# Kernel optimization log

Measured on AMD Instinct MI355X. Metric: run time of the kernel, lower is better.

The kernel has to match this reference:

```python
import jax, jax.numpy as jnp
import numpy as np

B, S, D, H = 2, 2048, 1024, 16
DK = D // H


def setup_inputs() -> dict:
    key = jax.random.key(0)
    ks = jax.random.split(key, 7)
    q = jax.random.normal(ks[0], (B, S, D), dtype=jnp.float32)
    k = jax.random.normal(ks[1], (B, S, D), dtype=jnp.float32)
    v = jax.random.normal(ks[2], (B, S, D), dtype=jnp.float32)
    # causal mask: mask==0 positions get -1e9 before softmax
    mask = jnp.tril(jnp.ones((S, S), dtype=jnp.int32))[None, None, :, :]
    scale = 0.02
    w_q = jax.random.normal(ks[3], (D, D), dtype=jnp.float32) * scale
    w_k = jax.random.normal(ks[4], (D, D), dtype=jnp.float32) * scale
    w_v = jax.random.normal(ks[5], (D, D), dtype=jnp.float32) * scale
    w_o = jax.random.normal(ks[6], (D, D), dtype=jnp.float32) * scale
    return {"q": q, "k": k, "v": v, "mask": mask,
            "w_q": w_q, "w_k": w_k, "w_v": w_v, "w_o": w_o}


def reference(q, k, v, mask, w_q, w_k, w_v, w_o):
    # nn.Linear(bias=False): x @ W.T
    query = q @ w_q.T  # [B,S,D]
    key = k @ w_k.T
    value = v @ w_v.T
    # split heads -> [B,H,S,DK]
    query = query.reshape(B, S, H, DK).transpose(0, 2, 1, 3)
    key = key.reshape(B, S, H, DK).transpose(0, 2, 1, 3)
    value = value.reshape(B, S, H, DK).transpose(0, 2, 1, 3)
    scores = jnp.einsum('bhqd,bhkd->bhqk', query, key) / jnp.sqrt(
        jnp.asarray(DK, dtype=query.dtype))
    scores = jnp.where(mask == 0, jnp.asarray(-1e9, scores.dtype), scores)
    attn = jax.nn.softmax(scores, axis=-1)  # dropout p=0.0 -> identity
    x = jnp.einsum('bhqk,bhkd->bhqd', attn, value)  # [B,H,S,DK]
    x = x.transpose(0, 2, 1, 3).reshape(B, S, D)
    return x @ w_o.T
```

## Files before the change

kernel.cpp:

```cpp
#include <hip/hip_runtime.h>

typedef __attribute__((ext_vector_type(8))) short short8;
typedef __attribute__((ext_vector_type(4))) float f32x4;

#define DEVI static __device__ __forceinline__

constexpr int BB = 2, SS = 2048, DD = 1024, HH = 16, DKK = 64;
constexpr size_t QN = (size_t)BB * SS * DD;
constexpr size_t WN = (size_t)DD * DD;

constexpr size_t OFF_WQ = 3 * QN;
constexpr size_t OFF_WO = OFF_WQ + 3 * WN;
constexpr size_t OFF_QM = OFF_WQ + 4 * WN;
constexpr size_t OFF_KM = OFF_QM + QN;
constexpr size_t OFF_VM = OFF_QM + 2 * QN;
constexpr size_t OFF_XC = OFF_QM + 3 * QN;

DEVI unsigned short f2bf(float f) {
  unsigned int u = __float_as_uint(f);
  u = (u + 0x7fffu + ((u >> 16) & 1u)) >> 16;
  return (unsigned short)u;
}

DEVI f32x4 fzero() { f32x4 z = {0.f, 0.f, 0.f, 0.f}; return z; }

DEVI void gld16(const void* g, void* l) {
  __builtin_amdgcn_global_load_lds((__attribute__((address_space(1))) void*)g,
                                   (__attribute__((address_space(3))) void*)l,
                                   16, 0, 0);
}

DEVI short8 mk8u(unsigned int a, unsigned int b, unsigned int c, unsigned int d) {
  union { short8 s; unsigned int u[4]; } x;
  x.u[0] = a; x.u[1] = b; x.u[2] = c; x.u[3] = d;
  return x.s;
}

DEVI short8 mk8q(unsigned long long lo, unsigned long long hi) {
  union { short8 s; unsigned long long q[2]; } x;
  x.q[0] = lo; x.q[1] = hi;
  return x.s;
}

DEVI unsigned int pkbf(float a, float b) {
  return __builtin_amdgcn_perm(__float_as_uint(b), __float_as_uint(a), 0x07060302u);
}

__global__ __launch_bounds__(256) void convert_all(
    const float* __restrict__ q, const float* __restrict__ k,
    const float* __restrict__ v, const float* __restrict__ wq,
    const float* __restrict__ wk, const float* __restrict__ wv,
    const float* __restrict__ wo, unsigned short* __restrict__ ws) {
  size_t t = (size_t)blockIdx.x * 256 + threadIdx.x;
  size_t e = t * 4;
  const float* src;
  size_t base, idx;
  if (e < 3 * QN) {
    size_t a = e >> 22;
    idx = e & (QN - 1);
    src = (a == 0) ? q : (a == 1) ? k : v;
    base = a * QN;
  } else {
    size_t r = e - 3 * QN;
    size_t a = r >> 20;
    idx = r & (WN - 1);
    src = (a == 0) ? wq : (a == 1) ? wk : (a == 2) ? wv : wo;
    base = 3 * QN + a * WN;
  }
  float4 f = *(const float4*)(src + idx);
  ushort4 o;
  o.x = f2bf(f.x); o.y = f2bf(f.y); o.z = f2bf(f.z); o.w = f2bf(f.w);
  *(ushort4*)(ws + base + idx) = o;
}

DEVI void gemm_tile_db(const unsigned short* __restrict__ A,
                       const unsigned short* __restrict__ Bw,
                       unsigned short* ldsA, unsigned short* ldsB,
                       int m0, int n0, f32x4 acc[4][4]) {
  const int tid = threadIdx.x;
  const int w = tid >> 6, l = tid & 63;
  const int lr = l & 15, qd = l >> 4;
  const int wr = w >> 1, wc = w & 1;

#pragma unroll
  for (int i = 0; i < 4; ++i)
#pragma unroll
    for (int j = 0; j < 4; ++j) acc[i][j] = fzero();

  const unsigned short* pa[4];
  const unsigned short* pb[4];
  int ls[4];
#pragma unroll
  for (int u = 0; u < 4; ++u) {
    int s = w * 4 + u;
    int t16 = s >> 1, kt = s & 1;
    pa[u] = A + (size_t)(m0 + t16 * 16 + lr) * DD + kt * 32 + qd * 8;
    pb[u] = Bw + (size_t)(n0 + t16 * 16 + lr) * DD + kt * 32 + qd * 8;
    ls[u] = s * 512;
  }

#pragma unroll
  for (int u = 0; u < 4; ++u) gld16(pa[u], ldsA + ls[u]);
#pragma unroll
  for (int u = 0; u < 4; ++u) gld16(pb[u], ldsB + ls[u]);

  constexpr int NIT = DD / 64;
#pragma unroll 1
  for (int it = 0; it < NIT; ++it) {
    __syncthreads();
    const int cur = (it & 1) * 8192;
    const int nxt = 8192 - cur;
    if (it + 1 < NIT) {
      const int k1 = (it + 1) * 64;
#pragma unroll
      for (int u = 0; u < 4; ++u) gld16(pa[u] + k1, ldsA + nxt + ls[u]);
#pragma unroll
      for (int u = 0; u < 4; ++u) gld16(pb[u] + k1, ldsB + nxt + ls[u]);
    }
#pragma unroll
    for (int ks = 0; ks < 2; ++ks) {
      short8 af[4], bf[4];
#pragma unroll
      for (int im = 0; im < 4; ++im)
        af[im] = *(const short8*)&ldsA[cur + ((wr * 4 + im) * 2 + ks) * 512 + l * 8];
#pragma unroll
      for (int in = 0; in < 4; ++in)
        bf[in] = *(const short8*)&ldsB[cur + ((wc * 4 + in) * 2 + ks) * 512 + l * 8];
#pragma unroll
      for (int im = 0; im < 4; ++im)
#pragma unroll
        for (int in = 0; in < 4; ++in)
          acc[im][in] = __builtin_amdgcn_mfma_f32_16x16x32_bf16(
              af[im], bf[in], acc[im][in], 0, 0, 0);
    }
  }
}

DEVI void gemm64_db(const unsigned short* __restrict__ A,
                    const unsigned short* __restrict__ Bw,
                    unsigned short* ldsA, unsigned short* ldsB,
                    int m0, int n0, f32x4 acc[4][2]) {
  const int tid = threadIdx.x;
  const int w = tid >> 6, l = tid & 63;
  const int lr = l & 15, qd = l >> 4;

#pragma unroll
  for (int i = 0; i < 4; ++i)
#pragma unroll
    for (int j = 0; j < 2; ++j) acc[i][j] = fzero();

  const unsigned short* pa[2];
  const unsigned short* pb[4];
  int lsa[2], lsb[4];
#pragma unroll
  for (int kh = 0; kh < 2; ++kh) {
    pa[kh] = A + (size_t)(m0 + w * 16 + lr) * DD + kh * 32 + qd * 8;
    lsa[kh] = (w * 2 + kh) * 512;
  }
#pragma unroll
  for (int r = 0; r < 2; ++r)
#pragma unroll
    for (int kh = 0; kh < 2; ++kh) {
      pb[r * 2 + kh] = Bw + (size_t)(n0 + (2 * w + r) * 16 + lr) * DD + kh * 32 + qd * 8;
      lsb[r * 2 + kh] = ((2 * w + r) * 2 + kh) * 512;
    }

#pragma unroll
  for (int u = 0; u < 2; ++u) gld16(pa[u], ldsA + lsa[u]);
#pragma unroll
  for (int u = 0; u < 4; ++u) gld16(pb[u], ldsB + lsb[u]);

  constexpr int NIT = DD / 64;
#pragma unroll 1
  for (int it = 0; it < NIT; ++it) {
    __syncthreads();
    const int curA = (it & 1) * 4096, curB = (it & 1) * 8192;
    if (it + 1 < NIT) {
      const int k1 = (it + 1) * 64;
      const int nxtA = 4096 - curA, nxtB = 8192 - curB;
#pragma unroll
      for (int u = 0; u < 2; ++u) gld16(pa[u] + k1, ldsA + nxtA + lsa[u]);
#pragma unroll
      for (int u = 0; u < 4; ++u) gld16(pb[u] + k1, ldsB + nxtB + lsb[u]);
    }
#pragma unroll
    for (int ks = 0; ks < 2; ++ks) {
      short8 af[4], bf[2];
#pragma unroll
      for (int im = 0; im < 4; ++im)
        af[im] = *(const short8*)&ldsA[curA + (im * 2 + ks) * 512 + l * 8];
#pragma unroll
      for (int in = 0; in < 2; ++in)
        bf[in] = *(const short8*)&ldsB[curB + ((2 * w + in) * 2 + ks) * 512 + l * 8];
#pragma unroll
      for (int im = 0; im < 4; ++im)
#pragma unroll
        for (int in = 0; in < 2; ++in)
          acc[im][in] = __builtin_amdgcn_mfma_f32_16x16x32_bf16(
              af[im], bf[in], acc[im][in], 0, 0, 0);
    }
  }
}

__global__ __launch_bounds__(256) void proj_gemm(unsigned short* __restrict__ ws) {
  __shared__ unsigned short ldsA[16384];
  __shared__ unsigned short ldsB[16384];
  const int z = blockIdx.z;
  const unsigned short* A = ws + (size_t)z * QN;
  const unsigned short* W = ws + OFF_WQ + (size_t)z * WN;
  unsigned short* O = ws + OFF_QM + (size_t)z * QN;
  const int m0 = blockIdx.x * 128, n0 = blockIdx.y * 128;
  f32x4 acc[4][4];
  gemm_tile_db(A, W, ldsA, ldsB, m0, n0, acc);

  const int tid = threadIdx.x;
  const int w = tid >> 6, l = tid & 63, lr = l & 15, qd = l >> 4;
  const int wr = w >> 1, wc = w & 1;
  if (z == 2) {
#pragma unroll
    for (int im = 0; im < 4; ++im)
#pragma unroll
      for (int in = 0; in < 4; ++in) {
        const int n = n0 + wc * 64 + in * 16 + lr;
        const int h = n >> 6, dk = n & 63;
        const int m = m0 + wr * 64 + im * 16 + qd * 4;
        const int b = m >> 11, s = m & 2047;
        ushort4 pk;
        pk.x = f2bf(acc[im][in][0]); pk.y = f2bf(acc[im][in][1]);
        pk.z = f2bf(acc[im][in][2]); pk.w = f2bf(acc[im][in][3]);
        *(ushort4*)&O[((size_t)(b * HH + h) * DKK + dk) * SS + s] = pk;
      }
  } else {
#pragma unroll
    for (int im = 0; im < 4; ++im)
#pragma unroll
      for (int in = 0; in < 4; ++in) {
        const int n = n0 + wc * 64 + in * 16 + lr;
        const int h = n >> 6, dk = n & 63;
#pragma unroll
        for (int i = 0; i < 4; ++i) {
          const int m = m0 + wr * 64 + im * 16 + qd * 4 + i;
          const int b = m >> 11, s = m & 2047;
          O[((size_t)(b * HH + h) * SS + s) * DKK + dk] = f2bf(acc[im][in][i]);
        }
      }
  }
}

__global__ __launch_bounds__(512) void flash_attn(
    const unsigned short* __restrict__ Qm, const unsigned short* __restrict__ Km,
    const unsigned short* __restrict__ Vt, unsigned short* __restrict__ Xc) {
  __shared__ unsigned short Kl[2][4096];
  __shared__ unsigned short Vl[2][4096];
  const int p = blockIdx.x, head = blockIdx.y, b = blockIdx.z;
  const int tid = threadIdx.x, w = tid >> 6, l = tid & 63, lr = l & 15, qd = l >> 4;
  const size_t bh = (size_t)(b * HH + head);
  const unsigned short* Qb = Qm + bh * SS * DKK;
  const unsigned short* Kb = Km + bh * SS * DKK;
  const unsigned short* Vb = Vt + bh * DKK * SS;

  const bool heavy = (w < 4);
  const int qt = heavy ? (31 - p) : p;
  const int nkv = 32 - p;
  const int qrow = qt * 64 + (w & 3) * 16 + lr;

  const int s0 = heavy ? w : (w - 4);
  const int s1 = s0 + 4;
  const int loOff = ((qd >> 1) * 16 + lr) * 8 + (qd & 1) * 4;
  const int hiOff = ((2 + (qd >> 1)) * 16 + lr) * 8 + (qd & 1) * 4;

  short8 qf0 = *(const short8*)&Qb[(size_t)qrow * DKK + qd * 8];
  short8 qf1 = *(const short8*)&Qb[(size_t)qrow * DKK + 32 + qd * 8];

  f32x4 o[4];
#pragma unroll
  for (int i = 0; i < 4; ++i) o[i] = fzero();
  float ll = 0.f;
  const float c1 = 0.18033688011112042f;
  const float mc = 8.0f * c1;

  {
    if (heavy) {
      gld16(&Kb[(size_t)((s0 >> 1) * 16 + lr) * DKK + (s0 & 1) * 32 + qd * 8],
            &Kl[0][s0 * 512]);
      gld16(&Kb[(size_t)((s1 >> 1) * 16 + lr) * DKK + (s1 & 1) * 32 + qd * 8],
            &Kl[0][s1 * 512]);
    } else {
      gld16(&Vb[(size_t)((s0 >> 1) * 16 + lr) * SS + (s0 & 1) * 32 + qd * 8],
            &Vl[0][s0 * 512]);
      gld16(&Vb[(size_t)((s1 >> 1) * 16 + lr) * SS + (s1 & 1) * 32 + qd * 8],
            &Vl[0][s1 * 512]);
    }
  }

#pragma unroll 1
  for (int kv = 0; kv < nkv; ++kv) {
    __syncthreads();
    const int cur = kv & 1;
    if (kv + 1 < nkv) {
      const int kv0n = (kv + 1) * 64;
      if (heavy) {
        gld16(&Kb[(size_t)(kv0n + (s0 >> 1) * 16 + lr) * DKK + (s0 & 1) * 32 + qd * 8],
              &Kl[cur ^ 1][s0 * 512]);
        gld16(&Kb[(size_t)(kv0n + (s1 >> 1) * 16 + lr) * DKK + (s1 & 1) * 32 + qd * 8],
              &Kl[cur ^ 1][s1 * 512]);
      } else {
        gld16(&Vb[(size_t)((s0 >> 1) * 16 + lr) * SS + kv0n + (s0 & 1) * 32 + qd * 8],
              &Vl[cur ^ 1][s0 * 512]);
        gld16(&Vb[(size_t)((s1 >> 1) * 16 + lr) * SS + kv0n + (s1 & 1) * 32 + qd * 8],
              &Vl[cur ^ 1][s1 * 512]);
      }
    }

    if (kv <= qt) {
      const int kv0 = kv * 64;
      f32x4 sc[4];
#pragma unroll
      for (int nt = 0; nt < 4; ++nt) {
        short8 kf0 = *(const short8*)&Kl[cur][(nt * 2 + 0) * 512 + l * 8];
        short8 kf1 = *(const short8*)&Kl[cur][(nt * 2 + 1) * 512 + l * 8];
        f32x4 zz = fzero();
        zz = __builtin_amdgcn_mfma_f32_16x16x32_bf16(kf0, qf0, zz, 0, 0, 0);
        sc[nt] = __builtin_amdgcn_mfma_f32_16x16x32_bf16(kf1, qf1, zz, 0, 0, 0);
      }
      if (kv == qt) {
#pragma unroll
        for (int nt = 0; nt < 4; ++nt)
#pragma unroll
          for (int i = 0; i < 4; ++i) {
            const int kvi = kv0 + nt * 16 + qd * 4 + i;
            if (kvi > qrow) sc[nt][i] = -3e38f;
          }
      }

      float rs = 0.f;
#pragma unroll
      for (int nt = 0; nt < 4; ++nt)
#pragma unroll
        for (int i = 0; i < 4; ++i) {
          const float pp = exp2f(fmaf(sc[nt][i], c1, -mc));
          sc[nt][i] = pp;
          rs += pp;
        }
      rs += __shfl_xor(rs, 16);
      rs += __shfl_xor(rs, 32);
      ll += rs;

      unsigned int pd[4][2];
#pragma unroll
      for (int f = 0; f < 4; ++f) {
        pd[f][0] = pkbf(sc[f][0], sc[f][1]);
        pd[f][1] = pkbf(sc[f][2], sc[f][3]);
      }

#pragma unroll
      for (int kh = 0; kh < 2; ++kh) {
        short8 bfr = mk8u(pd[2 * kh][0], pd[2 * kh][1],
                          pd[2 * kh + 1][0], pd[2 * kh + 1][1]);
#pragma unroll
        for (int mt = 0; mt < 4; ++mt) {
          const int sbase = (mt * 2 + kh) * 512;
          const unsigned long long lo =
              *(const unsigned long long*)&Vl[cur][sbase + loOff];
          const unsigned long long hi =
              *(const unsigned long long*)&Vl[cur][sbase + hiOff];
          o[mt] = __builtin_amdgcn_mfma_f32_16x16x32_bf16(mk8q(lo, hi), bfr,
                                                          o[mt], 0, 0, 0);
        }
      }
    }
  }

  const float inv = 1.0f / ll;
  unsigned short* Xr = Xc + ((size_t)b * SS + qrow) * DD + (size_t)head * DKK;
#pragma unroll
  for (int mt = 0; mt < 4; ++mt)
#pragma unroll
    for (int i = 0; i < 4; ++i)
      Xr[mt * 16 + qd * 4 + i] = f2bf(o[mt][i] * inv);
}

__global__ __launch_bounds__(256) void out_gemm(
    const unsigned short* __restrict__ Xc, const unsigned short* __restrict__ Wo,
    float* __restrict__ out) {
  __shared__ unsigned short ldsA[8192];
  __shared__ unsigned short ldsB[16384];
  const int m0 = blockIdx.x * 64, n0 = blockIdx.y * 128;
  f32x4 acc[4][2];
  gemm64_db(Xc, Wo, ldsA, ldsB, m0, n0, acc);

  const int tid = threadIdx.x;
  const int w = tid >> 6, l = tid & 63, lr = l & 15, qd = l >> 4;
#pragma unroll
  for (int im = 0; im < 4; ++im)
#pragma unroll
    for (int in = 0; in < 2; ++in) {
      const int n = n0 + w * 32 + in * 16 + lr;
#pragma unroll
      for (int i = 0; i < 4; ++i) {
        const int m = m0 + im * 16 + qd * 4 + i;
        out[(size_t)m * DD + n] = acc[im][in][i];
      }
    }
}

extern "C" void kernel_launch(void* const* d_in, const int* in_sizes, int n_in,
                              void* d_out, int out_size, void* d_ws, size_t ws_size,
                              hipStream_t stream) {
  (void)in_sizes; (void)n_in; (void)out_size; (void)ws_size;
  const float* q  = (const float*)d_in[0];
  const float* k  = (const float*)d_in[1];
  const float* v  = (const float*)d_in[2];
  const float* wq = (const float*)d_in[4];
  const float* wk = (const float*)d_in[5];
  const float* wv = (const float*)d_in[6];
  const float* wo = (const float*)d_in[7];
  unsigned short* ws = (unsigned short*)d_ws;
  float* out = (float*)d_out;

  convert_all<<<dim3(16384), dim3(256), 0, stream>>>(q, k, v, wq, wk, wv, wo, ws);
  proj_gemm<<<dim3(32, 8, 3), dim3(256), 0, stream>>>(ws);
  flash_attn<<<dim3(16, 16, 2), dim3(512), 0, stream>>>(ws + OFF_QM, ws + OFF_KM,
                                                        ws + OFF_VM, ws + OFF_XC);
  out_gemm<<<dim3(64, 8), dim3(256), 0, stream>>>(ws + OFF_XC, ws + OFF_WO, out);
}
```

Baseline: 252.6 us.

## Pair heavy/light query tiles per wave in flash attention; XCD-aware GEMM block remap

Attention blocks drop from 512 to 256 threads. Each wave now handles both a heavy (late) and a light (early) query tile, sharing each K/V LDS tile between the two MFMA streams instead of assigning them to separate waves. This balances causal work across waves and reuses K/V fragment loads, at the cost of higher register pressure and every wave loading both K and V. The projection and output GEMMs are also launched as 1D grids with an XCD-aware index remap, so blocks sharing A rows land on the same XCD for better L2 reuse.

```diff
diff --git a/kernel.cpp b/kernel.cpp
--- a/kernel.cpp
+++ b/kernel.cpp
@@ -205,11 +205,15 @@
 __global__ __launch_bounds__(256) void proj_gemm(unsigned short* __restrict__ ws) {
   __shared__ unsigned short ldsA[16384];
   __shared__ unsigned short ldsB[16384];
-  const int z = blockIdx.z;
+  const int idx = blockIdx.x;
+  const int z = idx >> 8;
+  const int r = idx & 255;
+  const int xcd = r & 7, t = r >> 3;
+  const int m0 = (xcd + 8 * (t & 3)) * 128;
+  const int n0 = (t >> 2) * 128;
   const unsigned short* A = ws + (size_t)z * QN;
   const unsigned short* W = ws + OFF_WQ + (size_t)z * WN;
   unsigned short* O = ws + OFF_QM + (size_t)z * QN;
-  const int m0 = blockIdx.x * 128, n0 = blockIdx.y * 128;
   f32x4 acc[4][4];
   gemm_tile_db(A, W, ldsA, ldsB, m0, n0, acc);
 
@@ -247,7 +251,7 @@
   }
 }
 
-__global__ __launch_bounds__(512) void flash_attn(
+__global__ __launch_bounds__(256) void flash_attn(
     const unsigned short* __restrict__ Qm, const unsigned short* __restrict__ Km,
     const unsigned short* __restrict__ Vt, unsigned short* __restrict__ Xc) {
   __shared__ unsigned short Kl[2][4096];
@@ -259,38 +263,36 @@
   const unsigned short* Kb = Km + bh * SS * DKK;
   const unsigned short* Vb = Vt + bh * DKK * SS;
 
-  const bool heavy = (w < 4);
-  const int qt = heavy ? (31 - p) : p;
+  const int qt_h = 31 - p;
   const int nkv = 32 - p;
-  const int qrow = qt * 64 + (w & 3) * 16 + lr;
-
-  const int s0 = heavy ? w : (w - 4);
-  const int s1 = s0 + 4;
+  const int qrow_h = qt_h * 64 + w * 16 + lr;
+  const int qrow_l = p * 64 + w * 16 + lr;
+
+  const int s0 = w, s1 = w + 4;
   const int loOff = ((qd >> 1) * 16 + lr) * 8 + (qd & 1) * 4;
   const int hiOff = ((2 + (qd >> 1)) * 16 + lr) * 8 + (qd & 1) * 4;
 
-  short8 qf0 = *(const short8*)&Qb[(size_t)qrow * DKK + qd * 8];
-  short8 qf1 = *(const short8*)&Qb[(size_t)qrow * DKK + 32 + qd * 8];
-
-  f32x4 o[4];
-#pragma unroll
-  for (int i = 0; i < 4; ++i) o[i] = fzero();
-  float ll = 0.f;
+  short8 qh0 = *(const short8*)&Qb[(size_t)qrow_h * DKK + qd * 8];
+  short8 qh1 = *(const short8*)&Qb[(size_t)qrow_h * DKK + 32 + qd * 8];
+  short8 ql0 = *(const short8*)&Qb[(size_t)qrow_l * DKK + qd * 8];
+  short8 ql1 = *(const short8*)&Qb[(size_t)qrow_l * DKK + 32 + qd * 8];
+
+  f32x4 oh[4], ol[4];
+#pragma unroll
+  for (int i = 0; i < 4; ++i) { oh[i] = fzero(); ol[i] = fzero(); }
+  float lh = 0.f, lt = 0.f;
   const float c1 = 0.18033688011112042f;
   const float mc = 8.0f * c1;
 
   {
-    if (heavy) {
-      gld16(&Kb[(size_t)((s0 >> 1) * 16 + lr) * DKK + (s0 & 1) * 32 + qd * 8],
-            &Kl[0][s0 * 512]);
-      gld16(&Kb[(size_t)((s1 >> 1) * 16 + lr) * DKK + (s1 & 1) * 32 + qd * 8],
-            &Kl[0][s1 * 512]);
-    } else {
-      gld16(&Vb[(size_t)((s0 >> 1) * 16 + lr) * SS + (s0 & 1) * 32 + qd * 8],
-            &Vl[0][s0 * 512]);
-      gld16(&Vb[(size_t)((s1 >> 1) * 16 + lr) * SS + (s1 & 1) * 32 + qd * 8],
-            &Vl[0][s1 * 512]);
-    }
+    gld16(&Kb[(size_t)((s0 >> 1) * 16 + lr) * DKK + (s0 & 1) * 32 + qd * 8],
+          &Kl[0][s0 * 512]);
+    gld16(&Kb[(size_t)((s1 >> 1) * 16 + lr) * DKK + (s1 & 1) * 32 + qd * 8],
+          &Kl[0][s1 * 512]);
+    gld16(&Vb[(size_t)((s0 >> 1) * 16 + lr) * SS + (s0 & 1) * 32 + qd * 8],
+          &Vl[0][s0 * 512]);
+    gld16(&Vb[(size_t)((s1 >> 1) * 16 + lr) * SS + (s1 & 1) * 32 + qd * 8],
+          &Vl[0][s1 * 512]);
   }
 
 #pragma unroll 1
@@ -299,64 +301,102 @@
     const int cur = kv & 1;
     if (kv + 1 < nkv) {
       const int kv0n = (kv + 1) * 64;
-      if (heavy) {
-        gld16(&Kb[(size_t)(kv0n + (s0 >> 1) * 16 + lr) * DKK + (s0 & 1) * 32 + qd * 8],
-              &Kl[cur ^ 1][s0 * 512]);
-        gld16(&Kb[(size_t)(kv0n + (s1 >> 1) * 16 + lr) * DKK + (s1 & 1) * 32 + qd * 8],
-              &Kl[cur ^ 1][s1 * 512]);
-      } else {
-        gld16(&Vb[(size_t)((s0 >> 1) * 16 + lr) * SS + kv0n + (s0 & 1) * 32 + qd * 8],
-              &Vl[cur ^ 1][s0 * 512]);
-        gld16(&Vb[(size_t)((s1 >> 1) * 16 + lr) * SS + kv0n + (s1 & 1) * 32 + qd * 8],
-              &Vl[cur ^ 1][s1 * 512]);
-      }
-    }
-
-    if (kv <= qt) {
-      const int kv0 = kv * 64;
-      f32x4 sc[4];
+      gld16(&Kb[(size_t)(kv0n + (s0 >> 1) * 16 + lr) * DKK + (s0 & 1) * 32 + qd * 8],
+            &Kl[cur ^ 1][s0 * 512]);
+      gld16(&Kb[(size_t)(kv0n + (s1 >> 1) * 16 + lr) * DKK + (s1 & 1) * 32 + qd * 8],
+            &Kl[cur ^ 1][s1 * 512]);
+      gld16(&Vb[(size_t)((s0 >> 1) * 16 + lr) * SS + kv0n + (s0 & 1) * 32 + qd * 8],
+            &Vl[cur ^ 1][s0 * 512]);
+      gld16(&Vb[(size_t)((s1 >> 1) * 16 + lr) * SS + kv0n + (s1 & 1) * 32 + qd * 8],
+            &Vl[cur ^ 1][s1 * 512]);
+    }
+
+    const int kv0 = kv * 64;
+    const bool lite = (kv <= p);
+    f32x4 sh[4], sl[4];
+    if (lite) {
 #pragma unroll
       for (int nt = 0; nt < 4; ++nt) {
         short8 kf0 = *(const short8*)&Kl[cur][(nt * 2 + 0) * 512 + l * 8];
         short8 kf1 = *(const short8*)&Kl[cur][(nt * 2 + 1) * 512 + l * 8];
-        f32x4 zz = fzero();
-        zz = __builtin_amdgcn_mfma_f32_16x16x32_bf16(kf0, qf0, zz, 0, 0, 0);
-        sc[nt] = __builtin_amdgcn_mfma_f32_16x16x32_bf16(kf1, qf1, zz, 0, 0, 0);
-      }
-      if (kv == qt) {
-#pragma unroll
-        for (int nt = 0; nt < 4; ++nt)
-#pragma unroll
-          for (int i = 0; i < 4; ++i) {
-            const int kvi = kv0 + nt * 16 + qd * 4 + i;
-            if (kvi > qrow) sc[nt][i] = -3e38f;
-          }
-      }
-
+        f32x4 z0 = __builtin_amdgcn_mfma_f32_16x16x32_bf16(kf0, qh0, fzero(), 0, 0, 0);
+        sh[nt] = __builtin_amdgcn_mfma_f32_16x16x32_bf16(kf1, qh1, z0, 0, 0, 0);
+        f32x4 z1 = __builtin_amdgcn_mfma_f32_16x16x32_bf16(kf0, ql0, fzero(), 0, 0, 0);
+        sl[nt] = __builtin_amdgcn_mfma_f32_16x16x32_bf16(kf1, ql1, z1, 0, 0, 0);
+      }
+    } else {
+#pragma unroll
+      for (int nt = 0; nt < 4; ++nt) {
+        short8 kf0 = *(const short8*)&Kl[cur][(nt * 2 + 0) * 512 + l * 8];
+        short8 kf1 = *(const short8*)&Kl[cur][(nt * 2 + 1) * 512 + l * 8];
+        f32x4 z0 = __builtin_amdgcn_mfma_f32_16x16x32_bf16(kf0, qh0, fzero(), 0, 0, 0);
+        sh[nt] = __builtin_amdgcn_mfma_f32_16x16x32_bf16(kf1, qh1, z0, 0, 0, 0);
+      }
+    }
+
+    if (kv == qt_h) {
+#pragma unroll
+      for (int nt = 0; nt < 4; ++nt)
+#pragma unroll
+        for (int i = 0; i < 4; ++i)
+          if (kv0 + nt * 16 + qd * 4 + i > qrow_h) sh[nt][i] = -3e38f;
+    }
+
+    unsigned int pdh[4][2];
+    {
       float rs = 0.f;
 #pragma unroll
       for (int nt = 0; nt < 4; ++nt)
 #pragma unroll
         for (int i = 0; i < 4; ++i) {
-          const float pp = exp2f(fmaf(sc[nt][i], c1, -mc));
-          sc[nt][i] = pp;
+          const float pp = exp2f(fmaf(sh[nt][i], c1, -mc));
+          sh[nt][i] = pp;
           rs += pp;
         }
       rs += __shfl_xor(rs, 16);
       rs += __shfl_xor(rs, 32);
-      ll += rs;
-
-      unsigned int pd[4][2];
+      lh += rs;
 #pragma unroll
       for (int f = 0; f < 4; ++f) {
-        pd[f][0] = pkbf(sc[f][0], sc[f][1]);
-        pd[f][1] = pkbf(sc[f][2], sc[f][3]);
-      }
-
+        pdh[f][0] = pkbf(sh[f][0], sh[f][1]);
+        pdh[f][1] = pkbf(sh[f][2], sh[f][3]);
+      }
+    }
+    unsigned int pdl[4][2];
+    if (lite) {
+      if (kv == p) {
+#pragma unroll
+        for (int nt = 0; nt < 4; ++nt)
+#pragma unroll
+          for (int i = 0; i < 4; ++i)
+            if (kv0 + nt * 16 + qd * 4 + i > qrow_l) sl[nt][i] = -3e38f;
+      }
+      float rs = 0.f;
+#pragma unroll
+      for (int nt = 0; nt < 4; ++nt)
+#pragma unroll
+        for (int i = 0; i < 4; ++i) {
+          const float pp = exp2f(fmaf(sl[nt][i], c1, -mc));
+          sl[nt][i] = pp;
+          rs += pp;
+        }
+      rs += __shfl_xor(rs, 16);
+      rs += __shfl_xor(rs, 32);
+      lt += rs;
+#pragma unroll
+      for (int f = 0; f < 4; ++f) {
+        pdl[f][0] = pkbf(sl[f][0], sl[f][1]);
+        pdl[f][1] = pkbf(sl[f][2], sl[f][3]);
+      }
+    }
+
+    if (lite) {
 #pragma unroll
       for (int kh = 0; kh < 2; ++kh) {
-        short8 bfr = mk8u(pd[2 * kh][0], pd[2 * kh][1],
-                          pd[2 * kh + 1][0], pd[2 * kh + 1][1]);
+        short8 bh_ = mk8u(pdh[2 * kh][0], pdh[2 * kh][1],
+                          pdh[2 * kh + 1][0], pdh[2 * kh + 1][1]);
+        short8 bl_ = mk8u(pdl[2 * kh][0], pdl[2 * kh][1],
+                          pdl[2 * kh + 1][0], pdl[2 * kh + 1][1]);
 #pragma unroll
         for (int mt = 0; mt < 4; ++mt) {
           const int sbase = (mt * 2 + kh) * 512;
@@ -364,20 +404,48 @@
               *(const unsigned long long*)&Vl[cur][sbase + loOff];
           const unsigned long long hi =
               *(const unsigned long long*)&Vl[cur][sbase + hiOff];
-          o[mt] = __builtin_amdgcn_mfma_f32_16x16x32_bf16(mk8q(lo, hi), bfr,
-                                                          o[mt], 0, 0, 0);
+          const short8 vf = mk8q(lo, hi);
+          oh[mt] = __builtin_amdgcn_mfma_f32_16x16x32_bf16(vf, bh_, oh[mt], 0, 0, 0);
+          ol[mt] = __builtin_amdgcn_mfma_f32_16x16x32_bf16(vf, bl_, ol[mt], 0, 0, 0);
         }
       }
-    }
-  }
-
-  const float inv = 1.0f / ll;
-  unsigned short* Xr = Xc + ((size_t)b * SS + qrow) * DD + (size_t)head * DKK;
-#pragma unroll
-  for (int mt = 0; mt < 4; ++mt)
-#pragma unroll
-    for (int i = 0; i < 4; ++i)
-      Xr[mt * 16 + qd * 4 + i] = f2bf(o[mt][i] * inv);
+    } else {
+#pragma unroll
+      for (int kh = 0; kh < 2; ++kh) {
+        short8 bh_ = mk8u(pdh[2 * kh][0], pdh[2 * kh][1],
+                          pdh[2 * kh + 1][0], pdh[2 * kh + 1][1]);
+#pragma unroll
+        for (int mt = 0; mt < 4; ++mt) {
+          const int sbase = (mt * 2 + kh) * 512;
+          const unsigned long long lo =
+              *(const unsigned long long*)&Vl[cur][sbase + loOff];
+          const unsigned long long hi =
+              *(const unsigned long long*)&Vl[cur][sbase + hiOff];
+          oh[mt] = __builtin_amdgcn_mfma_f32_16x16x32_bf16(mk8q(lo, hi), bh_,
+                                                           oh[mt], 0, 0, 0);
+        }
+      }
+    }
+  }
+
+  {
+    const float inv = 1.0f / lh;
+    unsigned short* Xr = Xc + ((size_t)b * SS + qrow_h) * DD + (size_t)head * DKK;
+#pragma unroll
+    for (int mt = 0; mt < 4; ++mt)
+#pragma unroll
+      for (int i = 0; i < 4; ++i)
+        Xr[mt * 16 + qd * 4 + i] = f2bf(oh[mt][i] * inv);
+  }
+  {
+    const float inv = 1.0f / lt;
+    unsigned short* Xr = Xc + ((size_t)b * SS + qrow_l) * DD + (size_t)head * DKK;
+#pragma unroll
+    for (int mt = 0; mt < 4; ++mt)
+#pragma unroll
+      for (int i = 0; i < 4; ++i)
+        Xr[mt * 16 + qd * 4 + i] = f2bf(ol[mt][i] * inv);
+  }
 }
 
 __global__ __launch_bounds__(256) void out_gemm(
@@ -385,7 +453,10 @@
     float* __restrict__ out) {
   __shared__ unsigned short ldsA[8192];
   __shared__ unsigned short ldsB[16384];
-  const int m0 = blockIdx.x * 64, n0 = blockIdx.y * 128;
+  const int idx = blockIdx.x;
+  const int xcd = idx & 7, t = idx >> 3;
+  const int m0 = (xcd + 8 * (t & 7)) * 64;
+  const int n0 = (t >> 3) * 128;
   f32x4 acc[4][2];
   gemm64_db(Xc, Wo, ldsA, ldsB, m0, n0, acc);
 
@@ -419,8 +490,8 @@
   float* out = (float*)d_out;
 
   convert_all<<<dim3(16384), dim3(256), 0, stream>>>(q, k, v, wq, wk, wv, wo, ws);
-  proj_gemm<<<dim3(32, 8, 3), dim3(256), 0, stream>>>(ws);
-  flash_attn<<<dim3(16, 16, 2), dim3(512), 0, stream>>>(ws + OFF_QM, ws + OFF_KM,
+  proj_gemm<<<dim3(768), dim3(256), 0, stream>>>(ws);
+  flash_attn<<<dim3(16, 16, 2), dim3(256), 0, stream>>>(ws + OFF_QM, ws + OFF_KM,
                                                         ws + OFF_VM, ws + OFF_XC);
-  out_gemm<<<dim3(64, 8), dim3(256), 0, stream>>>(ws + OFF_XC, ws + OFF_WO, out);
-}
+  out_gemm<<<dim3(512), dim3(256), 0, stream>>>(ws + OFF_XC, ws + OFF_WO, out);
+}
```

After: 268.0 us. 6.1% more time.
